# Performance work log

Hardware: AMD Instinct MI355X
Metric: run time of the kernel (lower is better)

Reference implementation:

```python
import jax, jax.numpy as jnp
import numpy as np

N_EXPERTS = 8
D_MODEL = 512
D_FF = 2048
TOP_P = 0.9
MIN_EXPERTS = 1
MAX_EXPERTS = 4
AUX_COEFF = 0.01
B, T = 4, 2048


def _top_p_routing(router_logits):
    # router_logits: (N, E)
    probs = jax.nn.softmax(router_logits, axis=-1)
    sorted_probs, sorted_idx = jax.lax.top_k(probs, MAX_EXPERTS)  # descending
    cumsum = jnp.cumsum(sorted_probs, axis=-1)
    shifted = jnp.concatenate([jnp.zeros_like(cumsum[:, :1]), cumsum[:, :-1]], axis=-1)
    slots = jnp.arange(MAX_EXPERTS)[None, :]
    keep = (slots < MIN_EXPERTS) | (shifted < TOP_P)  # (N, K) bool
    keep_f = keep.astype(probs.dtype)
    w = sorted_probs * keep_f
    idx = jnp.where(keep, sorted_idx, -1)
    wsum = jnp.maximum(w.sum(axis=-1, keepdims=True), 1e-9)
    w = (w / wsum) * keep_f
    return w, idx


def _aux_loss(router_logits, sel_idx):
    probs = jax.nn.softmax(router_logits, axis=-1)
    valid = (sel_idx >= 0)
    oh = jax.nn.one_hot(jnp.where(valid, sel_idx, 0), N_EXPERTS, dtype=probs.dtype)
    expert_mask = (oh * valid[..., None].astype(probs.dtype)).sum(axis=1)  # (N, E)
    total = jnp.maximum(expert_mask.sum(), 1.0)
    f_i = expert_mask.sum(axis=0) / total
    P_i = probs.mean(axis=0)
    return N_EXPERTS * (f_i * P_i).sum()


def _expert_ffn(x, W1, b1, W2, b2):
    # torch F.gelu default is exact erf gelu
    return jax.nn.gelu(x @ W1 + b1, approximate=False) @ W2 + b2


def setup_inputs() -> dict:
    key = jax.random.key(0)
    ks = jax.random.split(key, 6)
    x = jax.random.normal(ks[0], (B, T, D_MODEL), dtype=jnp.float32)
    router_w = jax.random.normal(ks[1], (D_MODEL, N_EXPERTS), dtype=jnp.float32) * 0.01
    W1 = jax.random.normal(ks[2], (N_EXPERTS, D_MODEL, D_FF), dtype=jnp.float32) * (1.0 / np.sqrt(D_MODEL))
    b1 = jax.random.normal(ks[3], (N_EXPERTS, D_FF), dtype=jnp.float32) * 0.01
    W2 = jax.random.normal(ks[4], (N_EXPERTS, D_FF, D_MODEL), dtype=jnp.float32) * (1.0 / np.sqrt(D_FF))
    b2 = jax.random.normal(ks[5], (N_EXPERTS, D_MODEL), dtype=jnp.float32) * 0.01
    return {"x": x, "router_w": router_w, "W1": W1, "b1": b1, "W2": W2, "b2": b2}


def reference(x, router_w, W1, b1, W2, b2):
    Bx, Tx, d = x.shape
    N = Bx * Tx
    x_flat = x.reshape(N, d)
    router_logits = x_flat @ router_w  # (N, E)
    sel_w, sel_idx = _top_p_routing(router_logits)  # (N, K), (N, K)

    out_flat = jnp.zeros((N, d), dtype=x.dtype)
    for e in range(N_EXPERTS):
        is_assigned = (sel_idx == e)
        # combine weight for expert e; exactly 0 for unassigned tokens,
        # so dense compute + weighted sum equals torch's masked gather/scatter.
        w_e = (sel_w * is_assigned.astype(sel_w.dtype)).sum(axis=-1)  # (N,)
        expert_out = _expert_ffn(x_flat, W1[e], b1[e], W2[e], b2[e])
        out_flat = out_flat + w_e[:, None] * expert_out

    output = out_flat.reshape(Bx, Tx, d)
    aux = AUX_COEFF * _aux_loss(router_logits, sel_idx)
    return output, aux
```

## Files before the change

kernel.cpp:

```cpp
#include <hip/hip_runtime.h>
#include <hip/hip_bf16.h>
#include <math.h>

#define NTOK 8192
#define DM 512
#define DFF 2048
#define NE 8
#define ROWCAP 33792

typedef __attribute__((ext_vector_type(8))) short bfrag;
typedef __attribute__((ext_vector_type(4))) float f32x4;
typedef __attribute__((ext_vector_type(4))) unsigned int u32x4;
typedef __attribute__((ext_vector_type(4))) short s16x4;

#define GLD_LDS16(gp, lp) __builtin_amdgcn_global_load_lds( \
    (const __attribute__((address_space(1))) void*)(gp),    \
    (__attribute__((address_space(3))) void*)(lp), 16, 0, 0)

#define LDS_OFF(p) ((unsigned)(size_t)(__attribute__((address_space(3))) void*)(p))

__device__ __forceinline__ void wg_barrier() {
  asm volatile("" ::: "memory");
  __builtin_amdgcn_sched_barrier(0);
  __builtin_amdgcn_s_barrier();
  __builtin_amdgcn_sched_barrier(0);
  asm volatile("" ::: "memory");
}

__device__ __forceinline__ bfrag lds_read_b128(unsigned addr) {
  bfrag r;
  asm volatile("ds_read_b128 %0, %1" : "=v"(r) : "v"(addr));
  return r;
}

__device__ __forceinline__ short f2bf(float f) {
  unsigned u = __builtin_bit_cast(unsigned, f);
  u += 0x7fffu + ((u >> 16) & 1u);
  return (short)(u >> 16);
}
__device__ __forceinline__ float bf2f(short s) {
  unsigned u = ((unsigned)(unsigned short)s) << 16;
  return __builtin_bit_cast(float, u);
}
__device__ __forceinline__ float fast_gelu(float v) {
  float u = fmaf(v * v * v, 0.044715f, v) * 0.7978845608f;
  float ex = __builtin_amdgcn_exp2f(u * -2.8853900818f);
  return v * __builtin_amdgcn_rcpf(1.f + ex);
}

__global__ __launch_bounds__(256) void cvt_kernel(const float* __restrict__ in,
                                                  short* __restrict__ o, int n4) {
  int i = blockIdx.x * 256 + threadIdx.x;
  if (i >= n4) return;
  f32x4 v = ((const f32x4*)in)[i];
  s16x4 s;
  #pragma unroll
  for (int j = 0; j < 4; j++) s[j] = f2bf(v[j]);
  ((s16x4*)o)[i] = s;
}

__global__ __launch_bounds__(256) void cvtT_kernel(const float* __restrict__ in,
                                                   short* __restrict__ o, int R, int C) {
  __shared__ float t[32][33];
  size_t eoff = (size_t)blockIdx.z * R * C;
  in += eoff; o += eoff;
  int r0 = blockIdx.x * 32, c0 = blockIdx.y * 32;
  int tx = threadIdx.x & 31, ty = threadIdx.x >> 5;
  #pragma unroll
  for (int i = 0; i < 32; i += 8)
    t[ty + i][tx] = in[(size_t)(r0 + ty + i) * C + c0 + tx];
  __syncthreads();
  #pragma unroll
  for (int i = 0; i < 32; i += 8)
    o[(size_t)(c0 + ty + i) * R + r0 + tx] = f2bf(t[tx][ty + i]);
}

__global__ __launch_bounds__(256) void router_kernel(const float* __restrict__ x,
                                                     const float* __restrict__ rw,
                                                     int* __restrict__ sel_e,
                                                     float* __restrict__ sel_w,
                                                     float* __restrict__ part) {
  __shared__ float s_cnt[NE], s_ps[NE];
  int tid = threadIdx.x;
  if (tid < NE) { s_cnt[tid] = 0.f; s_ps[tid] = 0.f; }
  __syncthreads();
  int wave = tid >> 6, lane = tid & 63;
  float myc[NE], myp[NE];
  #pragma unroll
  for (int e = 0; e < NE; e++) { myc[e] = 0.f; myp[e] = 0.f; }

  for (int i = 0; i < 8; i++) {
    int token = blockIdx.x * 32 + wave * 8 + i;
    const float* xt = x + (size_t)token * DM;
    float acc[NE];
    #pragma unroll
    for (int e = 0; e < NE; e++) acc[e] = 0.f;
    #pragma unroll
    for (int kk = 0; kk < DM / 64; kk++) {
      int k = kk * 64 + lane;
      float xv = xt[k];
      f32x4 r0 = *(const f32x4*)(rw + k * NE);
      f32x4 r1 = *(const f32x4*)(rw + k * NE + 4);
      acc[0] += xv * r0[0]; acc[1] += xv * r0[1]; acc[2] += xv * r0[2]; acc[3] += xv * r0[3];
      acc[4] += xv * r1[0]; acc[5] += xv * r1[1]; acc[6] += xv * r1[2]; acc[7] += xv * r1[3];
    }
    #pragma unroll
    for (int off = 32; off >= 1; off >>= 1) {
      #pragma unroll
      for (int e = 0; e < NE; e++) acc[e] += __shfl_xor(acc[e], off, 64);
    }
    float mx = acc[0];
    #pragma unroll
    for (int e = 1; e < NE; e++) mx = fmaxf(mx, acc[e]);
    float p[NE]; float sum = 0.f;
    #pragma unroll
    for (int e = 0; e < NE; e++) { p[e] = expf(acc[e] - mx); sum += p[e]; }
    float inv = 1.f / sum;
    #pragma unroll
    for (int e = 0; e < NE; e++) p[e] *= inv;
    float sp[4]; int si[4]; unsigned used = 0;
    #pragma unroll
    for (int s = 0; s < 4; s++) {
      float bp = -1.f; int bi = 0;
      #pragma unroll
      for (int e = 0; e < NE; e++)
        if (!((used >> e) & 1u) && p[e] > bp) { bp = p[e]; bi = e; }
      used |= 1u << bi; sp[s] = bp; si[s] = bi;
    }
    float csum = 0.f, wsum = 0.f; bool keep[4];
    #pragma unroll
    for (int s = 0; s < 4; s++) {
      keep[s] = (s < 1) || (csum < 0.9f);
      csum += sp[s];
      if (keep[s]) wsum += sp[s];
    }
    wsum = fmaxf(wsum, 1e-9f);
    if (lane == 0) {
      #pragma unroll
      for (int s = 0; s < 4; s++) {
        sel_e[token * 4 + s] = keep[s] ? si[s] : -1;
        sel_w[token * 4 + s] = keep[s] ? sp[s] / wsum : 0.f;
      }
      #pragma unroll
      for (int e = 0; e < NE; e++) myp[e] += p[e];
      #pragma unroll
      for (int s = 0; s < 4; s++) if (keep[s]) myc[si[s]] += 1.f;
    }
  }
  if (lane == 0) {
    #pragma unroll
    for (int e = 0; e < NE; e++) { atomicAdd(&s_cnt[e], myc[e]); atomicAdd(&s_ps[e], myp[e]); }
  }
  __syncthreads();
  if (tid < NE) {
    part[blockIdx.x * 16 + tid] = s_cnt[tid];
    part[blockIdx.x * 16 + 8 + tid] = s_ps[tid];
  }
}

__global__ void prep_kernel(const float* __restrict__ part, float* __restrict__ auxp,
                            int* __restrict__ meta) {
  __shared__ float red[16];
  int tid = threadIdx.x;
  if (tid < 16) {
    float s = 0.f;
    for (int b = 0; b < 256; b++) s += part[b * 16 + tid];
    red[tid] = s;
  }
  __syncthreads();
  if (tid == 0) {
    float tot = 0.f;
    for (int e = 0; e < NE; e++) tot += red[e];
    float t = fmaxf(tot, 1.f), s = 0.f;
    for (int e = 0; e < NE; e++) s += (red[e] / t) * (red[NE + e] / (float)NTOK);
    auxp[0] = 0.01f * (float)NE * s;
    int off = 0;
    for (int e = 0; e < NE; e++) {
      int c = (int)(red[e] + 0.5f);
      meta[e] = c; meta[8 + e] = off;
      off += (c + 127) & ~127;
    }
  }
  if (tid < NE) meta[16 + tid] = 0;
}

__global__ __launch_bounds__(256) void build_kernel(const int* __restrict__ sel_e,
                                                    const float* __restrict__ sel_w,
                                                    int* __restrict__ meta,
                                                    int* __restrict__ mlist,
                                                    float* __restrict__ wrow,
                                                    int* __restrict__ arow) {
  __shared__ int lcnt[NE], roff[NE];
  int tid = threadIdx.x;
  if (tid < NE) lcnt[tid] = 0;
  __syncthreads();
  int t = blockIdx.x * 32 + tid;
  int slots[4], es[4];
  bool active = tid < 32;
  if (active) {
    #pragma unroll
    for (int s = 0; s < 4; s++) {
      es[s] = sel_e[t * 4 + s];
      slots[s] = (es[s] >= 0) ? atomicAdd(&lcnt[es[s]], 1) : -1;
    }
  }
  __syncthreads();
  if (tid < NE) roff[tid] = atomicAdd(&meta[16 + tid], lcnt[tid]);
  __syncthreads();
  if (active) {
    #pragma unroll
    for (int s = 0; s < 4; s++) {
      int e = es[s];
      if (e >= 0) {
        int hrow = meta[8 + e] + roff[e] + slots[s];
        mlist[hrow] = t;
        wrow[hrow] = sel_w[t * 4 + s];
        arow[t * 4 + s] = hrow;
      } else {
        arow[t * 4 + s] = -1;
      }
    }
  }
}

__global__ __launch_bounds__(256, 2) void gemm1_sp(const short* __restrict__ A,
                                                   const short* __restrict__ W1t,
                                                   const float* __restrict__ b1,
                                                   short* __restrict__ H,
                                                   const int* __restrict__ mlist,
                                                   const int* __restrict__ meta) {
  __shared__ __align__(16) short As[2 * 128 * 64];
  __shared__ __align__(16) short Bs[2 * 128 * 64];
  int e = blockIdx.x >> 6, j = blockIdx.x & 63;
  int cnt = meta[e];
  if (j * 128 >= cnt) return;
  int base = meta[8 + e];
  int tid = threadIdx.x, wave = tid >> 6, lane = tid & 63;
  int wm = wave >> 1, wn = wave & 1, quad = lane >> 4, l16 = lane & 15;
  int n0 = blockIdx.y * 128;
  const short* Bt = W1t + (size_t)e * DFF * DM;

  const short* agp[4]; const short* bgp[4];
  #pragma unroll
  for (int q = 0; q < 4; q++) {
    int c = q * 256 + tid;
    int r = c >> 3, s = (c & 7) ^ (r & 7);
    int rl = j * 128 + r;
    int tok = mlist[base + (rl < cnt ? rl : cnt - 1)];
    agp[q] = A + (size_t)tok * DM + s * 8;
    bgp[q] = Bt + (size_t)(n0 + r) * DM + s * 8;
  }

  f32x4 acc[4][4];
  #pragma unroll
  for (int i = 0; i < 4; i++)
    #pragma unroll
    for (int jj = 0; jj < 4; jj++) acc[i][jj] = (f32x4){0.f, 0.f, 0.f, 0.f};

  auto stage = [&](int bsel, int kt) {
    short* Ab = As + bsel * 8192 + wave * 512;
    short* Bb = Bs + bsel * 8192 + wave * 512;
    #pragma unroll
    for (int q = 0; q < 4; q++) {
      GLD_LDS16(agp[q] + kt, Ab + q * 2048);
      GLD_LDS16(bgp[q] + kt, Bb + q * 2048);
    }
  };

  stage(0, 0);
  stage(1, 64);

  unsigned aAddr[4], bAddr[4];
  #pragma unroll
  for (int mi = 0; mi < 4; mi++) aAddr[mi] = LDS_OFF(As) + (wm * 64 + mi * 16 + l16) * 128;
  #pragma unroll
  for (int ni = 0; ni < 4; ni++) bAddr[ni] = LDS_OFF(Bs) + (wn * 64 + ni * 16 + l16) * 128;
  int swz = l16 & 7;
  unsigned soB[2];
  #pragma unroll
  for (int ks = 0; ks < 2; ks++) soB[ks] = (unsigned)((((ks << 2) | quad) ^ swz) << 4);

  const int NT = DM / 64;
  for (int t = 0; t < NT; t++) {
    if (t + 1 < NT) asm volatile("s_waitcnt vmcnt(8)" ::: "memory");
    else            asm volatile("s_waitcnt vmcnt(0)" ::: "memory");
    wg_barrier();
    unsigned bo = (unsigned)((t & 1) * 16384);
    #pragma unroll
    for (int ks = 0; ks < 2; ks++) {
      bfrag afr[4], bfr[4];
      #pragma unroll
      for (int mi = 0; mi < 4; mi++) afr[mi] = lds_read_b128(aAddr[mi] + bo + soB[ks]);
      #pragma unroll
      for (int ni = 0; ni < 4; ni++) bfr[ni] = lds_read_b128(bAddr[ni] + bo + soB[ks]);
      asm volatile("s_waitcnt lgkmcnt(0)" ::: "memory");
      __builtin_amdgcn_sched_barrier(0);
      __builtin_amdgcn_s_setprio(1);
      #pragma unroll
      for (int mi = 0; mi < 4; mi++)
        #pragma unroll
        for (int ni = 0; ni < 4; ni++)
          acc[mi][ni] = __builtin_amdgcn_mfma_f32_16x16x32_bf16(afr[mi], bfr[ni], acc[mi][ni], 0, 0, 0);
      __builtin_amdgcn_s_setprio(0);
    }
    wg_barrier();
    if (t + 2 < NT) stage(t & 1, (t + 2) * 64);
  }
  const float* bb = b1 + (size_t)e * DFF;
  #pragma unroll
  for (int mi = 0; mi < 4; mi++) {
    int rbase = base + j * 128 + wm * 64 + mi * 16 + quad * 4;
    #pragma unroll
    for (int ni = 0; ni < 4; ni++) {
      int col = n0 + wn * 64 + ni * 16 + l16;
      float bv = bb[col];
      #pragma unroll
      for (int r = 0; r < 4; r++)
        H[(size_t)(rbase + r) * DFF + col] = f2bf(fast_gelu(acc[mi][ni][r] + bv));
    }
  }
}

__global__ __launch_bounds__(256, 2) void gemm2_sp(const short* __restrict__ H,
                                                   const short* __restrict__ W2t,
                                                   const float* __restrict__ b2,
                                                   short* __restrict__ partial,
                                                   const float* __restrict__ wrow,
                                                   const int* __restrict__ meta) {
  __shared__ __align__(16) short As[2 * 128 * 64];
  __shared__ __align__(16) short Bs[2 * 128 * 64];
  int e = blockIdx.x >> 6, j = blockIdx.x & 63;
  int cnt = meta[e];
  if (j * 128 >= cnt) return;
  int base = meta[8 + e];
  int tid = threadIdx.x, wave = tid >> 6, lane = tid & 63;
  int wm = wave >> 1, wn = wave & 1, quad = lane >> 4, l16 = lane & 15;
  int n0 = blockIdx.y * 128;
  const short* Bt = W2t + (size_t)e * DM * DFF;

  const short* agp[4]; const short* bgp[4];
  #pragma unroll
  for (int q = 0; q < 4; q++) {
    int c = q * 256 + tid;
    int r = c >> 3, s = (c & 7) ^ (r & 7);
    agp[q] = H + (size_t)(base + j * 128 + r) * DFF + s * 8;
    bgp[q] = Bt + (size_t)(n0 + r) * DFF + s * 8;
  }

  f32x4 acc[4][4];
  #pragma unroll
  for (int i = 0; i < 4; i++)
    #pragma unroll
    for (int jj = 0; jj < 4; jj++) acc[i][jj] = (f32x4){0.f, 0.f, 0.f, 0.f};

  auto stage = [&](int bsel, int kt) {
    short* Ab = As + bsel * 8192 + wave * 512;
    short* Bb = Bs + bsel * 8192 + wave * 512;
    #pragma unroll
    for (int q = 0; q < 4; q++) {
      GLD_LDS16(agp[q] + kt, Ab + q * 2048);
      GLD_LDS16(bgp[q] + kt, Bb + q * 2048);
    }
  };

  stage(0, 0);
  stage(1, 64);

  unsigned aAddr[4], bAddr[4];
  #pragma unroll
  for (int mi = 0; mi < 4; mi++) aAddr[mi] = LDS_OFF(As) + (wm * 64 + mi * 16 + l16) * 128;
  #pragma unroll
  for (int ni = 0; ni < 4; ni++) bAddr[ni] = LDS_OFF(Bs) + (wn * 64 + ni * 16 + l16) * 128;
  int swz = l16 & 7;
  unsigned soB[2];
  #pragma unroll
  for (int ks = 0; ks < 2; ks++) soB[ks] = (unsigned)((((ks << 2) | quad) ^ swz) << 4);

  const int NT = DFF / 64;
  for (int t = 0; t < NT; t++) {
    if (t + 1 < NT) asm volatile("s_waitcnt vmcnt(8)" ::: "memory");
    else            asm volatile("s_waitcnt vmcnt(0)" ::: "memory");
    wg_barrier();
    unsigned bo = (unsigned)((t & 1) * 16384);
    #pragma unroll
    for (int ks = 0; ks < 2; ks++) {
      bfrag afr[4], bfr[4];
      #pragma unroll
      for (int mi = 0; mi < 4; mi++) afr[mi] = lds_read_b128(aAddr[mi] + bo + soB[ks]);
      #pragma unroll
      for (int ni = 0; ni < 4; ni++) bfr[ni] = lds_read_b128(bAddr[ni] + bo + soB[ks]);
      asm volatile("s_waitcnt lgkmcnt(0)" ::: "memory");
      __builtin_amdgcn_sched_barrier(0);
      __builtin_amdgcn_s_setprio(1);
      #pragma unroll
      for (int mi = 0; mi < 4; mi++)
        #pragma unroll
        for (int ni = 0; ni < 4; ni++)
          acc[mi][ni] = __builtin_amdgcn_mfma_f32_16x16x32_bf16(afr[mi], bfr[ni], acc[mi][ni], 0, 0, 0);
      __builtin_amdgcn_s_setprio(0);
    }
    wg_barrier();
    if (t + 2 < NT) stage(t & 1, (t + 2) * 64);
  }
  const float* bb = b2 + (size_t)e * DM;
  #pragma unroll
  for (int mi = 0; mi < 4; mi++) {
    int rbase = base + j * 128 + wm * 64 + mi * 16 + quad * 4;
    #pragma unroll
    for (int ni = 0; ni < 4; ni++) {
      int col = n0 + wn * 64 + ni * 16 + l16;
      float bv = bb[col];
      #pragma unroll
      for (int r = 0; r < 4; r++) {
        float w = wrow[rbase + r];
        partial[(size_t)(rbase + r) * DM + col] = f2bf(w * (acc[mi][ni][r] + bv));
      }
    }
  }
}

__global__ __launch_bounds__(256) void combine_kernel(const short* __restrict__ partial,
                                                      const int* __restrict__ arow,
                                                      float* __restrict__ out) {
  int gid = blockIdx.x * 256 + threadIdx.x;
  int t = gid >> 6, c0 = (gid & 63) << 3;
  const int* ar = arow + t * 4;
  float o[8];
  #pragma unroll
  for (int k = 0; k < 8; k++) o[k] = 0.f;
  #pragma unroll
  for (int s = 0; s < 4; s++) {
    int a = ar[s];
    if (a >= 0) {
      union { u32x4 v; short s16[8]; } buf;
      buf.v = *(const u32x4*)(partial + (size_t)a * DM + c0);
      #pragma unroll
      for (int k = 0; k < 8; k++) o[k] += bf2f(buf.s16[k]);
    }
  }
  float* op = out + (size_t)t * DM + c0;
  *(f32x4*)op = (f32x4){o[0], o[1], o[2], o[3]};
  *(f32x4*)(op + 4) = (f32x4){o[4], o[5], o[6], o[7]};
}

extern "C" void kernel_launch(void* const* d_in, const int* in_sizes, int n_in,
                              void* d_out, int out_size, void* d_ws, size_t ws_size,
                              hipStream_t stream) {
  const float* x  = (const float*)d_in[0];
  const float* rw = (const float*)d_in[1];
  const float* W1 = (const float*)d_in[2];
  const float* b1 = (const float*)d_in[3];
  const float* W2 = (const float*)d_in[4];
  const float* b2 = (const float*)d_in[5];
  float* out = (float*)d_out;

  char* base_p = (char*)d_ws; char* p = base_p;
  auto carve = [&](size_t bytes) { char* r = p; p += (bytes + 255) & ~(size_t)255; return r; };
  short* xb    = (short*)carve((size_t)NTOK * DM * 2);
  short* w1b   = (short*)carve((size_t)NE * DM * DFF * 2);
  short* w2b   = (short*)carve((size_t)NE * DFF * DM * 2);
  int*   sel_e = (int*)carve((size_t)NTOK * 4 * 4);
  float* sel_w = (float*)carve((size_t)NTOK * 4 * 4);
  float* part  = (float*)carve(256 * 16 * 4);
  int*   meta  = (int*)carve(64 * 4);
  int*   arow  = (int*)carve((size_t)NTOK * 4 * 4);
  int*   mlist = (int*)carve((size_t)ROWCAP * 4);
  float* wrow  = (float*)carve((size_t)ROWCAP * 4);
  short* Hbig  = (short*)carve((size_t)ROWCAP * DFF * 2);
  short* partial = (short*)carve((size_t)ROWCAP * DM * 2);

  cvt_kernel<<<(NTOK * DM / 4 + 255) / 256, 256, 0, stream>>>(x, xb, NTOK * DM / 4);
  cvtT_kernel<<<dim3(DM / 32, DFF / 32, NE), 256, 0, stream>>>(W1, w1b, DM, DFF);
  cvtT_kernel<<<dim3(DFF / 32, DM / 32, NE), 256, 0, stream>>>(W2, w2b, DFF, DM);
  router_kernel<<<256, 256, 0, stream>>>(x, rw, sel_e, sel_w, part);
  prep_kernel<<<1, 64, 0, stream>>>(part, out + (size_t)NTOK * DM, meta);
  build_kernel<<<256, 256, 0, stream>>>(sel_e, sel_w, meta, mlist, wrow, arow);
  gemm1_sp<<<dim3(NE * 64, DFF / 128), 256, 0, stream>>>(xb, w1b, b1, Hbig, mlist, meta);
  gemm2_sp<<<dim3(NE * 64, DM / 128), 256, 0, stream>>>(Hbig, w2b, b2, partial, wrow, meta);
  combine_kernel<<<NTOK * DM / 8 / 256, 256, 0, stream>>>(partial, arow, out);
}
```

Measured before the change: 426.4 us.

## Fuse x bf16 conversion into router, vectorize transpose stores, immediate LDS offsets

Removes the separate x-to-bf16 conversion kernel by writing the bf16 copy from the router kernel while it already reads x. The weight transpose kernel now writes four bf16 values per thread as one 8-byte store instead of scalar 2-byte stores. The prep reduction uses 256 threads with a two-level reduction instead of 16 serial loops. The GEMM inner loops use one base address with immediate ds_read offsets, cutting per-fragment address registers and VALU adds.

```diff
diff --git a/kernel.cpp b/kernel.cpp
--- a/kernel.cpp
+++ b/kernel.cpp
@@ -27,11 +27,8 @@
   asm volatile("" ::: "memory");
 }
 
-__device__ __forceinline__ bfrag lds_read_b128(unsigned addr) {
-  bfrag r;
-  asm volatile("ds_read_b128 %0, %1" : "=v"(r) : "v"(addr));
-  return r;
-}
+#define LDS_READ_OFF(dst, base, LIT) \
+  asm volatile("ds_read_b128 %0, %1 offset:" LIT : "=v"(dst) : "v"(base))
 
 __device__ __forceinline__ short f2bf(float f) {
   unsigned u = __builtin_bit_cast(unsigned, f);
@@ -46,17 +43,6 @@
   float u = fmaf(v * v * v, 0.044715f, v) * 0.7978845608f;
   float ex = __builtin_amdgcn_exp2f(u * -2.8853900818f);
   return v * __builtin_amdgcn_rcpf(1.f + ex);
-}
-
-__global__ __launch_bounds__(256) void cvt_kernel(const float* __restrict__ in,
-                                                  short* __restrict__ o, int n4) {
-  int i = blockIdx.x * 256 + threadIdx.x;
-  if (i >= n4) return;
-  f32x4 v = ((const f32x4*)in)[i];
-  s16x4 s;
-  #pragma unroll
-  for (int j = 0; j < 4; j++) s[j] = f2bf(v[j]);
-  ((s16x4*)o)[i] = s;
 }
 
 __global__ __launch_bounds__(256) void cvtT_kernel(const float* __restrict__ in,
@@ -70,13 +56,16 @@
   for (int i = 0; i < 32; i += 8)
     t[ty + i][tx] = in[(size_t)(r0 + ty + i) * C + c0 + tx];
   __syncthreads();
-  #pragma unroll
-  for (int i = 0; i < 32; i += 8)
-    o[(size_t)(c0 + ty + i) * R + r0 + tx] = f2bf(t[tx][ty + i]);
+  int tx4 = threadIdx.x & 7, oc = threadIdx.x >> 3;
+  s16x4 v;
+  #pragma unroll
+  for (int jj = 0; jj < 4; jj++) v[jj] = f2bf(t[tx4 * 4 + jj][oc]);
+  *(s16x4*)(o + (size_t)(c0 + oc) * R + r0 + tx4 * 4) = v;
 }
 
 __global__ __launch_bounds__(256) void router_kernel(const float* __restrict__ x,
                                                      const float* __restrict__ rw,
+                                                     short* __restrict__ xb,
                                                      int* __restrict__ sel_e,
                                                      float* __restrict__ sel_w,
                                                      float* __restrict__ part) {
@@ -99,6 +88,7 @@
     for (int kk = 0; kk < DM / 64; kk++) {
       int k = kk * 64 + lane;
       float xv = xt[k];
+      xb[(size_t)token * DM + k] = f2bf(xv);
       f32x4 r0 = *(const f32x4*)(rw + k * NE);
       f32x4 r1 = *(const f32x4*)(rw + k * NE + 4);
       acc[0] += xv * r0[0]; acc[1] += xv * r0[1]; acc[2] += xv * r0[2]; acc[3] += xv * r0[3];
@@ -158,22 +148,31 @@
   }
 }
 
-__global__ void prep_kernel(const float* __restrict__ part, float* __restrict__ auxp,
-                            int* __restrict__ meta) {
+__global__ __launch_bounds__(256) void prep_kernel(const float* __restrict__ part,
+                                                   float* __restrict__ auxp,
+                                                   int* __restrict__ meta) {
+  __shared__ float red2[16][16];
   __shared__ float red[16];
   int tid = threadIdx.x;
+  int idx = tid & 15, g = tid >> 4;
+  float s = 0.f;
+  #pragma unroll
+  for (int b = 0; b < 16; b++) s += part[(g * 16 + b) * 16 + idx];
+  red2[g][idx] = s;
+  __syncthreads();
   if (tid < 16) {
-    float s = 0.f;
-    for (int b = 0; b < 256; b++) s += part[b * 16 + tid];
-    red[tid] = s;
+    float t = 0.f;
+    #pragma unroll
+    for (int g2 = 0; g2 < 16; g2++) t += red2[g2][tid];
+    red[tid] = t;
   }
   __syncthreads();
   if (tid == 0) {
     float tot = 0.f;
     for (int e = 0; e < NE; e++) tot += red[e];
-    float t = fmaxf(tot, 1.f), s = 0.f;
-    for (int e = 0; e < NE; e++) s += (red[e] / t) * (red[NE + e] / (float)NTOK);
-    auxp[0] = 0.01f * (float)NE * s;
+    float t = fmaxf(tot, 1.f), s2 = 0.f;
+    for (int e = 0; e < NE; e++) s2 += (red[e] / t) * (red[NE + e] / (float)NTOK);
+    auxp[0] = 0.01f * (float)NE * s2;
     int off = 0;
     for (int e = 0; e < NE; e++) {
       int c = (int)(red[e] + 0.5f);
@@ -270,15 +269,11 @@
   stage(0, 0);
   stage(1, 64);
 
-  unsigned aAddr[4], bAddr[4];
-  #pragma unroll
-  for (int mi = 0; mi < 4; mi++) aAddr[mi] = LDS_OFF(As) + (wm * 64 + mi * 16 + l16) * 128;
-  #pragma unroll
-  for (int ni = 0; ni < 4; ni++) bAddr[ni] = LDS_OFF(Bs) + (wn * 64 + ni * 16 + l16) * 128;
-  int swz = l16 & 7;
+  unsigned aAddr0 = LDS_OFF(As) + (wm * 64 + l16) * 128;
+  unsigned bAddr0 = LDS_OFF(Bs) + (wn * 64 + l16) * 128;
   unsigned soB[2];
   #pragma unroll
-  for (int ks = 0; ks < 2; ks++) soB[ks] = (unsigned)((((ks << 2) | quad) ^ swz) << 4);
+  for (int ks = 0; ks < 2; ks++) soB[ks] = (unsigned)((((ks << 2) | quad) ^ (l16 & 7)) << 4);
 
   const int NT = DM / 64;
   for (int t = 0; t < NT; t++) {
@@ -288,11 +283,13 @@
     unsigned bo = (unsigned)((t & 1) * 16384);
     #pragma unroll
     for (int ks = 0; ks < 2; ks++) {
+      unsigned aB = aAddr0 + bo + soB[ks];
+      unsigned bB = bAddr0 + bo + soB[ks];
       bfrag afr[4], bfr[4];
-      #pragma unroll
-      for (int mi = 0; mi < 4; mi++) afr[mi] = lds_read_b128(aAddr[mi] + bo + soB[ks]);
-      #pragma unroll
-      for (int ni = 0; ni < 4; ni++) bfr[ni] = lds_read_b128(bAddr[ni] + bo + soB[ks]);
+      LDS_READ_OFF(afr[0], aB, "0");    LDS_READ_OFF(afr[1], aB, "2048");
+      LDS_READ_OFF(afr[2], aB, "4096"); LDS_READ_OFF(afr[3], aB, "6144");
+      LDS_READ_OFF(bfr[0], bB, "0");    LDS_READ_OFF(bfr[1], bB, "2048");
+      LDS_READ_OFF(bfr[2], bB, "4096"); LDS_READ_OFF(bfr[3], bB, "6144");
       asm volatile("s_waitcnt lgkmcnt(0)" ::: "memory");
       __builtin_amdgcn_sched_barrier(0);
       __builtin_amdgcn_s_setprio(1);
@@ -366,15 +363,11 @@
   stage(0, 0);
   stage(1, 64);
 
-  unsigned aAddr[4], bAddr[4];
-  #pragma unroll
-  for (int mi = 0; mi < 4; mi++) aAddr[mi] = LDS_OFF(As) + (wm * 64 + mi * 16 + l16) * 128;
-  #pragma unroll
-  for (int ni = 0; ni < 4; ni++) bAddr[ni] = LDS_OFF(Bs) + (wn * 64 + ni * 16 + l16) * 128;
-  int swz = l16 & 7;
+  unsigned aAddr0 = LDS_OFF(As) + (wm * 64 + l16) * 128;
+  unsigned bAddr0 = LDS_OFF(Bs) + (wn * 64 + l16) * 128;
   unsigned soB[2];
   #pragma unroll
-  for (int ks = 0; ks < 2; ks++) soB[ks] = (unsigned)((((ks << 2) | quad) ^ swz) << 4);
+  for (int ks = 0; ks < 2; ks++) soB[ks] = (unsigned)((((ks << 2) | quad) ^ (l16 & 7)) << 4);
 
   const int NT = DFF / 64;
   for (int t = 0; t < NT; t++) {
@@ -384,11 +377,13 @@
     unsigned bo = (unsigned)((t & 1) * 16384);
     #pragma unroll
     for (int ks = 0; ks < 2; ks++) {
+      unsigned aB = aAddr0 + bo + soB[ks];
+      unsigned bB = bAddr0 + bo + soB[ks];
       bfrag afr[4], bfr[4];
-      #pragma unroll
-      for (int mi = 0; mi < 4; mi++) afr[mi] = lds_read_b128(aAddr[mi] + bo + soB[ks]);
-      #pragma unroll
-      for (int ni = 0; ni < 4; ni++) bfr[ni] = lds_read_b128(bAddr[ni] + bo + soB[ks]);
+      LDS_READ_OFF(afr[0], aB, "0");    LDS_READ_OFF(afr[1], aB, "2048");
+      LDS_READ_OFF(afr[2], aB, "4096"); LDS_READ_OFF(afr[3], aB, "6144");
+      LDS_READ_OFF(bfr[0], bB, "0");    LDS_READ_OFF(bfr[1], bB, "2048");
+      LDS_READ_OFF(bfr[2], bB, "4096"); LDS_READ_OFF(bfr[3], bB, "6144");
       asm volatile("s_waitcnt lgkmcnt(0)" ::: "memory");
       __builtin_amdgcn_sched_barrier(0);
       __builtin_amdgcn_s_setprio(1);
@@ -469,11 +464,10 @@
   short* Hbig  = (short*)carve((size_t)ROWCAP * DFF * 2);
   short* partial = (short*)carve((size_t)ROWCAP * DM * 2);
 
-  cvt_kernel<<<(NTOK * DM / 4 + 255) / 256, 256, 0, stream>>>(x, xb, NTOK * DM / 4);
   cvtT_kernel<<<dim3(DM / 32, DFF / 32, NE), 256, 0, stream>>>(W1, w1b, DM, DFF);
   cvtT_kernel<<<dim3(DFF / 32, DM / 32, NE), 256, 0, stream>>>(W2, w2b, DFF, DM);
-  router_kernel<<<256, 256, 0, stream>>>(x, rw, sel_e, sel_w, part);
-  prep_kernel<<<1, 64, 0, stream>>>(part, out + (size_t)NTOK * DM, meta);
+  router_kernel<<<256, 256, 0, stream>>>(x, rw, xb, sel_e, sel_w, part);
+  prep_kernel<<<1, 256, 0, stream>>>(part, out + (size_t)NTOK * DM, meta);
   build_kernel<<<256, 256, 0, stream>>>(sel_e, sel_w, meta, mlist, wrow, arow);
   gemm1_sp<<<dim3(NE * 64, DFF / 128), 256, 0, stream>>>(xb, w1b, b1, Hbig, mlist, meta);
   gemm2_sp<<<dim3(NE * 64, DM / 128), 256, 0, stream>>>(Hbig, w2b, b2, partial, wrow, meta);
```

Measured after the change: 429.4 us. Within noise of the previous version (+0.7%).
